# Kernel optimization log

Measured on AMD Instinct MI355X. Metric: run time of the kernel, lower is better.

Reference implementation:

```python
import jax, jax.numpy as jnp
import numpy as np

B, S, D = 4, 2048, 1024  # batch, seq_len, model dim (= qk_dim = output_dim)


def setup_inputs() -> dict:
    key = jax.random.key(0)
    kq, kk, kv, kwq, kwk, kwv = jax.random.split(key, 6)
    q = jax.random.normal(kq, (B, S, D), dtype=jnp.float32)
    k = jax.random.normal(kk, (B, S, D), dtype=jnp.float32)
    v = jax.random.normal(kv, (B, S, D), dtype=jnp.float32)
    # causal mask, broadcast over batch
    mask = jnp.broadcast_to(jnp.tril(jnp.ones((S, S), dtype=bool)), (B, S, S))
    W_q = jax.random.uniform(kwq, (D, D), dtype=jnp.float32)
    W_k = jax.random.uniform(kwk, (D, D), dtype=jnp.float32)
    W_v = jax.random.uniform(kwv, (D, D), dtype=jnp.float32)
    return {"q": q, "k": k, "v": v, "mask": mask, "W_q": W_q, "W_k": W_k, "W_v": W_v}


def reference(q, k, v, mask, W_q, W_k, W_v):
    q1 = q @ W_q  # (B, S, D)
    k1 = k @ W_k  # (B, S, D)
    v1 = v @ W_v  # (B, S, D)
    qk = jnp.einsum('bij,bkj->bik', q1, k1)  # (B, S, S)
    qk = qk * jax.lax.rsqrt(float(k1.shape[-1]))
    neg_inf = jnp.finfo(jnp.float32).min
    qk = jnp.where(mask, qk, neg_inf)
    s = jax.nn.softmax(qk, axis=-1)
    return jnp.einsum('bij,bjk->bik', s, v1)
```

## Files before the change

kernel.cpp:

```cpp
#include <hip/hip_runtime.h>
#include <hip/hip_bf16.h>
#include <float.h>


typedef __attribute__((ext_vector_type(8))) short bf16x8;
typedef __attribute__((ext_vector_type(4))) float f32x4;

#define MFMA16 __builtin_amdgcn_mfma_f32_16x16x32_bf16

union U8 { bf16x8 v; unsigned w[4]; };

__device__ __forceinline__ ushort f2bf(float x) {
  union { float f; unsigned u; } v; v.f = x;
  unsigned r = v.u + 0x7fffu + ((v.u >> 16) & 1u);
  return (ushort)(r >> 16);
}
__device__ __forceinline__ float bf2f(ushort h) {
  union { unsigned u; float f; } v; v.u = ((unsigned)h) << 16;
  return v.f;
}
__device__ __forceinline__ void splitf(float x, ushort& hi, ushort& lo) {
  hi = f2bf(x);
  lo = f2bf(x - bf2f(hi));
}

__device__ __forceinline__ bf16x8 cvt8(const float* lp) {
  U8 H;
#pragma unroll
  for (int p = 0; p < 4; ++p) {
    const unsigned u0 = __float_as_uint(lp[2 * p]);
    const unsigned u1 = __float_as_uint(lp[2 * p + 1]);
    const unsigned r0 = (u0 + 0x7fffu + ((u0 >> 16) & 1u)) >> 16;
    const unsigned r1 = (u1 + 0x7fffu + ((u1 >> 16) & 1u)) & 0xffff0000u;
    H.w[p] = r0 | r1;
  }
  return H.v;
}

#define GLOAD16(gp, lp)                                                        \
  __builtin_amdgcn_global_load_lds(                                            \
      (const __attribute__((address_space(1))) void*)(gp),                     \
      (__attribute__((address_space(3))) void*)(lp), 16, 0, 0)

__device__ __forceinline__ void stage_bf16_32(const ushort* g, int pitch,
                                              ushort* lds, int w, int lane) {
#pragma unroll
  for (int i = 0; i < 2; ++i) {
    const int c = w * 2 + i;
    const int row = c * 16 + (lane >> 2);
    const int kp = (lane & 3) * 8;
    GLOAD16(g + (size_t)row * pitch + kp, lds + c * 512);
  }
}
__device__ __forceinline__ void stage_bf16_64(const ushort* g, int pitch,
                                              ushort* lds, int w, int lane) {
#pragma unroll
  for (int i = 0; i < 4; ++i) {
    const int c = w * 4 + i;
    const int row = c * 8 + (lane >> 3);
    const int kp = (lane & 7) * 8;
    GLOAD16(g + (size_t)row * pitch + kp, lds + c * 512);
  }
}
__device__ __forceinline__ void stage_bf16_64x64(const ushort* g, int pitch,
                                                 ushort* lds, int w, int lane) {
#pragma unroll
  for (int i = 0; i < 2; ++i) {
    const int c = w * 2 + i;
    const int row = c * 8 + (lane >> 3);
    const int kp = (lane & 7) * 8;
    GLOAD16(g + (size_t)row * pitch + kp, lds + c * 512);
  }
}
__device__ __forceinline__ void stage_f32_32(const float* g, int pitch,
                                             float* lds, int w, int lane) {
#pragma unroll
  for (int i = 0; i < 4; ++i) {
    const int c = w * 4 + i;
    const int row = c * 8 + (lane >> 3);
    const int kp = (lane & 7) * 4;
    GLOAD16(g + (size_t)row * pitch + kp, lds + c * 256);
  }
}

__global__ __launch_bounds__(256) void wt_split(
    const float* __restrict__ q, const float* __restrict__ k,
    const float* __restrict__ W0, const float* __restrict__ W1,
    const float* __restrict__ W2, ushort* __restrict__ Th0,
    ushort* __restrict__ Tl0, ushort* __restrict__ Th1,
    ushort* __restrict__ Tl1, ushort* __restrict__ Th2,
    ushort* __restrict__ qh, ushort* __restrict__ ql,
    ushort* __restrict__ kh, ushort* __restrict__ kl) {
  __shared__ float t[32][33];
  const int f = blockIdx.x;
  if (f < 3072) {
    const int z = f >> 10, r10 = f & 1023;
    const int bx = r10 & 31, by = r10 >> 5;
    const float* W = z == 0 ? W0 : (z == 1 ? W1 : W2);
    ushort* Th = z == 0 ? Th0 : (z == 1 ? Th1 : Th2);
    ushort* Tl = z == 0 ? Tl0 : (z == 1 ? Tl1 : nullptr);
    const int r = threadIdx.x >> 3, c4 = (threadIdx.x & 7) * 4;
    const float4 x = *reinterpret_cast<const float4*>(
        &W[(size_t)(bx * 32 + r) * 1024 + by * 32 + c4]);
    t[r][c4] = x.x; t[r][c4 + 1] = x.y; t[r][c4 + 2] = x.z; t[r][c4 + 3] = x.w;
    __syncthreads();
    ushort h[4], l[4];
#pragma unroll
    for (int j = 0; j < 4; ++j) splitf(t[c4 + j][r], h[j], l[j]);
    const size_t o = (size_t)(by * 32 + r) * 1024 + bx * 32 + c4;
    *reinterpret_cast<ushort4*>(&Th[o]) = ushort4{h[0], h[1], h[2], h[3]};
    if (Tl)
      *reinterpret_cast<ushort4*>(&Tl[o]) = ushort4{l[0], l[1], l[2], l[3]};
  } else {
    const int fl = f - 3072;
    const float* X = (fl >> 11) ? k : q;
    ushort* H = (fl >> 11) ? kh : qh;
    ushort* L = (fl >> 11) ? kl : ql;
    const int n4 = 2097152;
    for (int i = (fl & 2047) * 256 + threadIdx.x; i < n4; i += 2048 * 256) {
      const float4 x = reinterpret_cast<const float4*>(X)[i];
      ushort h0, l0, h1, l1, h2, l2, h3, l3;
      splitf(x.x, h0, l0); splitf(x.y, h1, l1);
      splitf(x.z, h2, l2); splitf(x.w, h3, l3);
      reinterpret_cast<ushort4*>(H)[i] = ushort4{h0, h1, h2, h3};
      reinterpret_cast<ushort4*>(L)[i] = ushort4{l0, l1, l2, l3};
    }
  }
}

__global__ __launch_bounds__(256) void proj_qk(
    const ushort* __restrict__ Ah0, const ushort* __restrict__ Al0,
    const ushort* __restrict__ Ah1, const ushort* __restrict__ Al1,
    const ushort* __restrict__ Bh0, const ushort* __restrict__ Bl0,
    const ushort* __restrict__ Bh1, const ushort* __restrict__ Bl1,
    ushort* __restrict__ Oh0, ushort* __restrict__ Ol0,
    ushort* __restrict__ Oh1, ushort* __restrict__ Ol1) {
  __shared__ ushort Ahs[4096], Als[4096], Bhs[4096], Bls[4096];
  const int f = blockIdx.x;
  const int xb = (f >> 3) & 7;
  const int r = (f & 7) + ((f >> 6) << 3);
  const int yb = r & 63, z = r >> 6;
  const ushort* Ah = z ? Ah1 : Ah0;
  const ushort* Al = z ? Al1 : Al0;
  const ushort* Bh = z ? Bh1 : Bh0;
  const ushort* Bl = z ? Bl1 : Bl0;
  ushort* Oh = z ? Oh1 : Oh0;
  ushort* Ol = z ? Ol1 : Ol0;
  const int tid = threadIdx.x, lane = tid & 63, w = tid >> 6;
  const int wr = w >> 1, wc = w & 1;
  const int lr = lane & 15, kg = lane >> 4;
  const int m0 = yb * 128, n0 = xb * 128;
  f32x4 acc[4][4] = {};

  for (int k0 = 0; k0 < 1024; k0 += 32) {
    stage_bf16_32(Ah + (size_t)m0 * 1024 + k0, 1024, Ahs, w, lane);
    stage_bf16_32(Al + (size_t)m0 * 1024 + k0, 1024, Als, w, lane);
    stage_bf16_32(Bh + (size_t)n0 * 1024 + k0, 1024, Bhs, w, lane);
    stage_bf16_32(Bl + (size_t)n0 * 1024 + k0, 1024, Bls, w, lane);
    __syncthreads();
    bf16x8 ah[4], al[4], bh[4], bl[4];
#pragma unroll
    for (int m = 0; m < 4; ++m) {
      ah[m] = *reinterpret_cast<bf16x8*>(&Ahs[(wr * 64 + m * 16 + lr) * 32 + kg * 8]);
      al[m] = *reinterpret_cast<bf16x8*>(&Als[(wr * 64 + m * 16 + lr) * 32 + kg * 8]);
    }
#pragma unroll
    for (int n = 0; n < 4; ++n) {
      bh[n] = *reinterpret_cast<bf16x8*>(&Bhs[(wc * 64 + n * 16 + lr) * 32 + kg * 8]);
      bl[n] = *reinterpret_cast<bf16x8*>(&Bls[(wc * 64 + n * 16 + lr) * 32 + kg * 8]);
    }
#pragma unroll
    for (int m = 0; m < 4; ++m)
#pragma unroll
      for (int n = 0; n < 4; ++n) {
        acc[m][n] = MFMA16(ah[m], bh[n], acc[m][n], 0, 0, 0);
        acc[m][n] = MFMA16(ah[m], bl[n], acc[m][n], 0, 0, 0);
        acc[m][n] = MFMA16(al[m], bh[n], acc[m][n], 0, 0, 0);
      }
    __syncthreads();
  }
#pragma unroll
  for (int m = 0; m < 4; ++m)
#pragma unroll
    for (int n = 0; n < 4; ++n)
#pragma unroll
      for (int reg = 0; reg < 4; ++reg) {
        const int gm = m0 + wr * 64 + m * 16 + kg * 4 + reg;
        const int gn = n0 + wc * 64 + n * 16 + lr;
        ushort h, l;
        splitf(acc[m][n][reg], h, l);
        Oh[(size_t)gm * 1024 + gn] = h;
        Ol[(size_t)gm * 1024 + gn] = l;
      }
}

__global__ __launch_bounds__(256) void qk2(
    const ushort* __restrict__ q1h, const ushort* __restrict__ q1l,
    const ushort* __restrict__ k1h, const ushort* __restrict__ k1l,
    float* __restrict__ scoresA, float* __restrict__ scoresB) {
  __shared__ ushort Ahs[4096], Als[4096], Bhs[4096], Bls[4096];
  const int f = blockIdx.x;
  const int s = (f & 7) * 136 + (f >> 3);
  const int z = s / 544;
  const int rem = s % 544;
  const int b = rem / 136;
  int p = rem % 136, ti = 0, accp = 0;
  while (accp + ti + 1 <= p) { accp += ti + 1; ++ti; }
  const int tj = p - accp;
  const int tid = threadIdx.x, lane = tid & 63, w = tid >> 6;
  const int wr = w >> 1, wc = w & 1;
  const int lr = lane & 15, kg = lane >> 4;
  const int kh0 = z * 512;
  const ushort* qh = q1h + ((size_t)b * 2048 + ti * 128) * 1024 + kh0;
  const ushort* ql = q1l + ((size_t)b * 2048 + ti * 128) * 1024 + kh0;
  const ushort* kh = k1h + ((size_t)b * 2048 + tj * 128) * 1024 + kh0;
  const ushort* kl = k1l + ((size_t)b * 2048 + tj * 128) * 1024 + kh0;
  f32x4 acc[4][4] = {};

  for (int k0 = 0; k0 < 512; k0 += 32) {
    stage_bf16_32(qh + k0, 1024, Ahs, w, lane);
    stage_bf16_32(ql + k0, 1024, Als, w, lane);
    stage_bf16_32(kh + k0, 1024, Bhs, w, lane);
    stage_bf16_32(kl + k0, 1024, Bls, w, lane);
    __syncthreads();
    bf16x8 ah[4], al[4], bh[4], bl[4];
#pragma unroll
    for (int m = 0; m < 4; ++m) {
      ah[m] = *reinterpret_cast<bf16x8*>(&Ahs[(wr * 64 + m * 16 + lr) * 32 + kg * 8]);
      al[m] = *reinterpret_cast<bf16x8*>(&Als[(wr * 64 + m * 16 + lr) * 32 + kg * 8]);
    }
#pragma unroll
    for (int n = 0; n < 4; ++n) {
      bh[n] = *reinterpret_cast<bf16x8*>(&Bhs[(wc * 64 + n * 16 + lr) * 32 + kg * 8]);
      bl[n] = *reinterpret_cast<bf16x8*>(&Bls[(wc * 64 + n * 16 + lr) * 32 + kg * 8]);
    }
#pragma unroll
    for (int m = 0; m < 4; ++m)
#pragma unroll
      for (int n = 0; n < 4; ++n) {
        acc[m][n] = MFMA16(ah[m], bh[n], acc[m][n], 0, 0, 0);
        acc[m][n] = MFMA16(ah[m], bl[n], acc[m][n], 0, 0, 0);
        acc[m][n] = MFMA16(al[m], bh[n], acc[m][n], 0, 0, 0);
      }
    __syncthreads();
  }
  const float sc = 0.03125f;
  float* st = (z ? scoresB : scoresA) + ((size_t)b * 136 + p) * 16384;
#pragma unroll
  for (int m = 0; m < 4; ++m)
#pragma unroll
    for (int n = 0; n < 4; ++n)
#pragma unroll
      for (int reg = 0; reg < 4; ++reg) {
        const int il = wr * 64 + m * 16 + kg * 4 + reg;
        const int jl = wc * 64 + n * 16 + lr;
        st[il * 128 + jl] = acc[m][n][reg] * sc;
      }
}

__global__ __launch_bounds__(256) void sm_projv(
    float* __restrict__ scoresA, const float* __restrict__ scoresB,
    const ushort* __restrict__ Wvt, const float* __restrict__ V,
    ushort* __restrict__ v1t) {
  __shared__ __align__(16) char smem[24576];
  const int tid = threadIdx.x, lane = tid & 63, w = tid >> 6;
  const int fg = blockIdx.x;
  if (fg < 8192) {
    float* red = reinterpret_cast<float*>(smem);
    const int b = fg >> 11, r = fg & 2047;
    const int ti = r >> 7, rl = r & 127, ncol = (ti + 1) * 128;
    const int valid = r + 1;
    const size_t tbase = ((size_t)b * 136 + (ti * (ti + 1)) / 2) * 16384;
    float* srowA = scoresA + tbase;
    const float* srowB = scoresB + tbase;

    float vals[2][4];
    float mx = -FLT_MAX;
#pragma unroll
    for (int c = 0; c < 2; ++c) {
      const int j = tid * 4 + c * 1024;
      const size_t o = (size_t)(j >> 7) * 16384 + rl * 128 + (j & 127);
      const float4 a = *reinterpret_cast<const float4*>(srowA + o);
      const float4 bb = *reinterpret_cast<const float4*>(srowB + o);
      vals[c][0] = (j + 0 < valid) ? a.x + bb.x : -FLT_MAX;
      vals[c][1] = (j + 1 < valid) ? a.y + bb.y : -FLT_MAX;
      vals[c][2] = (j + 2 < valid) ? a.z + bb.z : -FLT_MAX;
      vals[c][3] = (j + 3 < valid) ? a.w + bb.w : -FLT_MAX;
      mx = fmaxf(mx, fmaxf(fmaxf(vals[c][0], vals[c][1]),
                           fmaxf(vals[c][2], vals[c][3])));
    }
#pragma unroll
    for (int o = 32; o; o >>= 1) mx = fmaxf(mx, __shfl_xor(mx, o));
    if (lane == 0) red[w] = mx;
    __syncthreads();
    mx = fmaxf(fmaxf(red[0], red[1]), fmaxf(red[2], red[3]));

    float ex[2][4];
    float sum = 0.f;
#pragma unroll
    for (int c = 0; c < 2; ++c)
#pragma unroll
      for (int e = 0; e < 4; ++e) {
        const int j = tid * 4 + c * 1024 + e;
        ex[c][e] = (j < valid) ? __expf(vals[c][e] - mx) : 0.f;
        sum += ex[c][e];
      }
#pragma unroll
    for (int o = 32; o; o >>= 1) sum += __shfl_xor(sum, o);
    if (lane == 0) red[4 + w] = sum;
    __syncthreads();
    sum = red[4] + red[5] + red[6] + red[7];
    const float inv = 1.f / sum;
#pragma unroll
    for (int c = 0; c < 2; ++c) {
      const int j = tid * 4 + c * 1024;
      if (j < ncol) {
        ushort* pt =
            reinterpret_cast<ushort*>(srowA + (size_t)(j >> 7) * 16384);
        ushort4 pw;
        pw.x = f2bf(ex[c][0] * inv); pw.y = f2bf(ex[c][1] * inv);
        pw.z = f2bf(ex[c][2] * inv); pw.w = f2bf(ex[c][3] * inv);
        *reinterpret_cast<ushort4*>(&pt[rl * 256 + (j & 127)]) = pw;
      }
    }
  } else {
    ushort* Ahs = reinterpret_cast<ushort*>(smem);
    float* Bs = reinterpret_cast<float*>(smem + 8192);
    const int f2 = fg - 8192;
    const int yb = (f2 >> 3) & 7;
    const int xb = (f2 & 7) + ((f2 >> 6) << 3);
    const int wr = w >> 1, wc = w & 1;
    const int lr = lane & 15, kg = lane >> 4;
    const int m0 = yb * 128;
    const int n0 = xb * 128;
    f32x4 acc[4][4] = {};

    for (int k0 = 0; k0 < 1024; k0 += 32) {
      stage_bf16_32(Wvt + (size_t)m0 * 1024 + k0, 1024, Ahs, w, lane);
      stage_f32_32(V + (size_t)n0 * 1024 + k0, 1024, Bs, w, lane);
      __syncthreads();
      bf16x8 ah[4], bh[4];
#pragma unroll
      for (int m = 0; m < 4; ++m)
        ah[m] = *reinterpret_cast<bf16x8*>(
            &Ahs[(wr * 64 + m * 16 + lr) * 32 + kg * 8]);
#pragma unroll
      for (int n = 0; n < 4; ++n)
        bh[n] = cvt8(&Bs[(wc * 64 + n * 16 + lr) * 32 + kg * 8]);
#pragma unroll
      for (int m = 0; m < 4; ++m)
#pragma unroll
        for (int n = 0; n < 4; ++n)
          acc[m][n] = MFMA16(ah[m], bh[n], acc[m][n], 0, 0, 0);
      __syncthreads();
    }
#pragma unroll
    for (int m = 0; m < 4; ++m)
#pragma unroll
      for (int n = 0; n < 4; ++n)
#pragma unroll
        for (int reg = 0; reg < 4; ++reg) {
          const int gm = m0 + wr * 64 + m * 16 + kg * 4 + reg;
          const int gn = n0 + wc * 64 + n * 16 + lr;
          const int b = gn >> 11, jj = gn & 2047;
          v1t[((size_t)b << 21) + (size_t)gm * 2048 + jj] = f2bf(acc[m][n][reg]);
        }
  }
}

__global__ __launch_bounds__(256) void pv2(const float* __restrict__ scores,
                                           const ushort* __restrict__ v1t,
                                           float* __restrict__ out) {
  __shared__ ushort Ps[128 * 64], Vs[64 * 64];
  const int fl = blockIdx.x;
  const int s = (fl & 7) * 128 + (fl >> 3);
  const int b = s >> 8, rem = s & 255;
  const int ti = 15 - (rem >> 4);
  const int n0 = (rem & 15) * 64;
  const int tid = threadIdx.x, lane = tid & 63, w = tid >> 6;
  const int wr = w >> 1, wc = w & 1;
  const int lr = lane & 15, kg = lane >> 4;
  const int tri_ti = (ti * (ti + 1)) / 2;
  const ushort* vbase = v1t + ((size_t)b << 21) + (size_t)n0 * 2048;
  const int kend = (ti + 1) * 128;
  f32x4 acc[4][2] = {};

  for (int k0 = 0; k0 < kend; k0 += 64) {
    const ushort* pt = reinterpret_cast<const ushort*>(
        scores + ((size_t)b * 136 + tri_ti + (k0 >> 7)) * 16384);
    stage_bf16_64(pt + (k0 & 64), 256, Ps, w, lane);
    stage_bf16_64x64(vbase + k0, 2048, Vs, w, lane);
    __syncthreads();
#pragma unroll
    for (int t2 = 0; t2 < 2; ++t2) {
      bf16x8 pa[4], vb[2];
#pragma unroll
      for (int m = 0; m < 4; ++m)
        pa[m] = *reinterpret_cast<bf16x8*>(
            &Ps[(wr * 64 + m * 16 + lr) * 64 + t2 * 32 + kg * 8]);
#pragma unroll
      for (int n = 0; n < 2; ++n)
        vb[n] = *reinterpret_cast<bf16x8*>(
            &Vs[(wc * 32 + n * 16 + lr) * 64 + t2 * 32 + kg * 8]);
#pragma unroll
      for (int m = 0; m < 4; ++m)
#pragma unroll
        for (int n = 0; n < 2; ++n)
          acc[m][n] = MFMA16(pa[m], vb[n], acc[m][n], 0, 0, 0);
    }
    __syncthreads();
  }
#pragma unroll
  for (int m = 0; m < 4; ++m)
#pragma unroll
    for (int n = 0; n < 2; ++n)
#pragma unroll
      for (int reg = 0; reg < 4; ++reg) {
        const int gm = ti * 128 + wr * 64 + m * 16 + kg * 4 + reg;
        const int gn = n0 + wc * 32 + n * 16 + lr;
        out[((size_t)b * 2048 + gm) * 1024 + gn] = acc[m][n][reg];
      }
}

extern "C" void kernel_launch(void* const* d_in, const int* in_sizes, int n_in,
                              void* d_out, int out_size, void* d_ws,
                              size_t ws_size, hipStream_t stream) {
  const float* q = (const float*)d_in[0];
  const float* k = (const float*)d_in[1];
  const float* v = (const float*)d_in[2];
  const float* Wq = (const float*)d_in[4];
  const float* Wk = (const float*)d_in[5];
  const float* Wv = (const float*)d_in[6];
  float* out = (float*)d_out;

  char* ws = (char*)d_ws;
  const size_t SCORES_T = 35651584;
  float* scoresA = (float*)ws;
  float* scoresB = (float*)(ws + SCORES_T);
  ushort* qsh = (ushort*)ws;
  ushort* qsl = qsh + 8388608;
  ushort* ksh = qsh + 2 * 8388608;
  ushort* ksl = qsh + 3 * 8388608;
  ushort* q1hi = (ushort*)(ws + 2 * SCORES_T);
  ushort* q1lo = q1hi + 8388608;
  ushort* k1hi = q1hi + 2 * 8388608;
  ushort* k1lo = q1hi + 3 * 8388608;
  ushort* v1t = (ushort*)(ws + 2 * SCORES_T);
  ushort* Wqth = (ushort*)(ws + 2 * SCORES_T + 67108864);
  ushort* Wqtl = Wqth + 1048576;
  ushort* Wkth = Wqth + 2097152;
  ushort* Wktl = Wqth + 3145728;
  ushort* Wvt  = Wqth + 4194304;
  const size_t need = 2 * SCORES_T + 67108864 + 10485760;
  if (ws_size < need) return;

  dim3 blk(256);
  wt_split<<<dim3(7168), blk, 0, stream>>>(q, k, Wq, Wk, Wv, Wqth, Wqtl, Wkth,
                                           Wktl, Wvt, qsh, qsl, ksh, ksl);
  proj_qk<<<dim3(1024), blk, 0, stream>>>(qsh, qsl, ksh, ksl, Wqth, Wqtl,
                                          Wkth, Wktl, q1hi, q1lo, k1hi, k1lo);
  qk2<<<dim3(1088), blk, 0, stream>>>(q1hi, q1lo, k1hi, k1lo, scoresA,
                                      scoresB);
  sm_projv<<<dim3(8704), blk, 0, stream>>>(scoresA, scoresB, Wvt, v, v1t);
  pv2<<<dim3(1024), blk, 0, stream>>>(scoresA, v1t, out);
}
```

Before: 312.6 us.

## Rewrite Q/K projection GEMM as 256x256 double-buffered 8-wave pipelined kernel

Replaces the 128x128, 4-wave projection GEMM with a 256x256-tile, 512-thread kernel. It streams the three split-bf16 products (hi*hi, lo*hi, hi*lo) as three sequential K segments through double-buffered, XOR-swizzled LDS using async global-to-LDS loads. Staging is interleaved with MFMA quadrants under fine-grained barriers, vmcnt waits and raised wave priority, to overlap memory traffic with compute and cut redundant operand loads. The cost is a much larger LDS footprint (two waves-per-SIMD target) and fewer blocks (256), which may underfill the CUs. Correctness also depends on the hand-placed waitcnt and barrier ordering.

```diff
diff --git a/kernel.cpp b/kernel.cpp
--- a/kernel.cpp
+++ b/kernel.cpp
@@ -42,6 +42,9 @@
       (const __attribute__((address_space(1))) void*)(gp),                     \
       (__attribute__((address_space(3))) void*)(lp), 16, 0, 0)
 
+#define BARRIER() asm volatile("s_barrier" ::: "memory")
+#define VMCNT4() asm volatile("s_waitcnt vmcnt(4)" ::: "memory")
+
 __device__ __forceinline__ void stage_bf16_32(const ushort* g, int pitch,
                                               ushort* lds, int w, int lane) {
 #pragma unroll
@@ -80,6 +83,18 @@
     const int row = c * 8 + (lane >> 3);
     const int kp = (lane & 7) * 4;
     GLOAD16(g + (size_t)row * pitch + kp, lds + c * 256);
+  }
+}
+
+__device__ __forceinline__ void stage_half8(const ushort* __restrict__ g,
+                                            ushort* lds, int k0, int t) {
+#pragma unroll
+  for (int i = 0; i < 2; ++i) {
+    const int c = t + i * 512;
+    const int row = c >> 3;
+    const int pcb = (c & 7) * 16;
+    const int lcb = pcb ^ (((row >> 2) & 3) << 5);
+    GLOAD16(g + (size_t)row * 1024 + k0 + (lcb >> 1), lds + c * 8);
   }
 }
 
@@ -128,65 +143,136 @@
   }
 }
 
-__global__ __launch_bounds__(256) void proj_qk(
+__global__ __launch_bounds__(512, 2) void proj_qk8(
     const ushort* __restrict__ Ah0, const ushort* __restrict__ Al0,
     const ushort* __restrict__ Ah1, const ushort* __restrict__ Al1,
     const ushort* __restrict__ Bh0, const ushort* __restrict__ Bl0,
     const ushort* __restrict__ Bh1, const ushort* __restrict__ Bl1,
     ushort* __restrict__ Oh0, ushort* __restrict__ Ol0,
     ushort* __restrict__ Oh1, ushort* __restrict__ Ol1) {
-  __shared__ ushort Ahs[4096], Als[4096], Bhs[4096], Bls[4096];
-  const int f = blockIdx.x;
-  const int xb = (f >> 3) & 7;
-  const int r = (f & 7) + ((f >> 6) << 3);
-  const int yb = r & 63, z = r >> 6;
+  __shared__ ushort As[2][16384];
+  __shared__ ushort Bs[2][16384];
+  const int bid = blockIdx.x;
+  const int fid = (bid & 7) * 32 + (bid >> 3);
+  const int z = fid >> 7, r = fid & 127;
+  const int yt = r >> 2, xt = r & 3;
   const ushort* Ah = z ? Ah1 : Ah0;
   const ushort* Al = z ? Al1 : Al0;
   const ushort* Bh = z ? Bh1 : Bh0;
   const ushort* Bl = z ? Bl1 : Bl0;
   ushort* Oh = z ? Oh1 : Oh0;
   ushort* Ol = z ? Ol1 : Ol0;
-  const int tid = threadIdx.x, lane = tid & 63, w = tid >> 6;
-  const int wr = w >> 1, wc = w & 1;
+  const size_t am0 = (size_t)yt * 256 * 1024;
+  const size_t bn0 = (size_t)xt * 256 * 1024;
+  const int t = threadIdx.x;
+  const int lane = t & 63, w = t >> 6;
+  const int wm = w >> 2, wn = w & 3;
   const int lr = lane & 15, kg = lane >> 4;
-  const int m0 = yb * 128, n0 = xb * 128;
-  f32x4 acc[4][4] = {};
-
-  for (int k0 = 0; k0 < 1024; k0 += 32) {
-    stage_bf16_32(Ah + (size_t)m0 * 1024 + k0, 1024, Ahs, w, lane);
-    stage_bf16_32(Al + (size_t)m0 * 1024 + k0, 1024, Als, w, lane);
-    stage_bf16_32(Bh + (size_t)n0 * 1024 + k0, 1024, Bhs, w, lane);
-    stage_bf16_32(Bl + (size_t)n0 * 1024 + k0, 1024, Bls, w, lane);
-    __syncthreads();
-    bf16x8 ah[4], al[4], bh[4], bl[4];
-#pragma unroll
-    for (int m = 0; m < 4; ++m) {
-      ah[m] = *reinterpret_cast<bf16x8*>(&Ahs[(wr * 64 + m * 16 + lr) * 32 + kg * 8]);
-      al[m] = *reinterpret_cast<bf16x8*>(&Als[(wr * 64 + m * 16 + lr) * 32 + kg * 8]);
-    }
-#pragma unroll
-    for (int n = 0; n < 4; ++n) {
-      bh[n] = *reinterpret_cast<bf16x8*>(&Bhs[(wc * 64 + n * 16 + lr) * 32 + kg * 8]);
-      bl[n] = *reinterpret_cast<bf16x8*>(&Bls[(wc * 64 + n * 16 + lr) * 32 + kg * 8]);
-    }
+  f32x4 acc[8][4] = {};
+  bf16x8 Ar[4][2], Br[4][2];
+
+  auto stage_unit = [&](int kt, int u) {
+    if (kt >= 48) kt -= 48;
+    const int seg = kt >> 4;
+    const int k0 = (kt & 15) * 64;
+    const int slot = kt & 1;
+    const int h = u & 1;
+    if (u < 2) {
+      const ushort* g = ((seg == 1) ? Al : Ah) + am0 + (size_t)(h * 128) * 1024;
+      stage_half8(g, &As[slot][h * 8192], k0, t);
+    } else {
+      const ushort* g = ((seg == 2) ? Bl : Bh) + bn0 + (size_t)(h * 128) * 1024;
+      stage_half8(g, &Bs[slot][h * 8192], k0, t);
+    }
+  };
+  auto loadA = [&](int slot, int mq) {
 #pragma unroll
     for (int m = 0; m < 4; ++m)
 #pragma unroll
-      for (int n = 0; n < 4; ++n) {
-        acc[m][n] = MFMA16(ah[m], bh[n], acc[m][n], 0, 0, 0);
-        acc[m][n] = MFMA16(ah[m], bl[n], acc[m][n], 0, 0, 0);
-        acc[m][n] = MFMA16(al[m], bh[n], acc[m][n], 0, 0, 0);
-      }
-    __syncthreads();
-  }
-#pragma unroll
-  for (int m = 0; m < 4; ++m)
+      for (int ks = 0; ks < 2; ++ks) {
+        const int row = wm * 128 + (mq * 4 + m) * 16 + lr;
+        const int cb = (ks * 64 + kg * 16) ^ (((row >> 2) & 3) << 5);
+        Ar[m][ks] =
+            *reinterpret_cast<const bf16x8*>(&As[slot][row * 64 + (cb >> 1)]);
+      }
+  };
+  auto loadB = [&](int slot, int nq) {
+#pragma unroll
+    for (int n = 0; n < 2; ++n)
+#pragma unroll
+      for (int ks = 0; ks < 2; ++ks) {
+        const int col = wn * 64 + (nq * 2 + n) * 16 + lr;
+        const int cb = (ks * 64 + kg * 16) ^ (((col >> 2) & 3) << 5);
+        Br[nq * 2 + n][ks] =
+            *reinterpret_cast<const bf16x8*>(&Bs[slot][col * 64 + (cb >> 1)]);
+      }
+  };
+  auto mfma_q = [&](int mq, int nq) {
+    __builtin_amdgcn_s_setprio(1);
+#pragma unroll
+    for (int m = 0; m < 4; ++m)
+#pragma unroll
+      for (int n = 0; n < 2; ++n)
+#pragma unroll
+        for (int ks = 0; ks < 2; ++ks)
+          acc[mq * 4 + m][nq * 2 + n] = MFMA16(
+              Ar[m][ks], Br[nq * 2 + n][ks], acc[mq * 4 + m][nq * 2 + n], 0, 0, 0);
+    __builtin_amdgcn_s_setprio(0);
+  };
+
+  stage_unit(0, 0); stage_unit(0, 1); stage_unit(0, 2); stage_unit(0, 3);
+  stage_unit(1, 0);
+
+  for (int it = 0; it < 24; ++it) {
+    const int kt1 = 2 * it + 1;
+    stage_unit(kt1, 1);
+    VMCNT4(); BARRIER();
+    loadA(0, 0); loadB(0, 0);
+    mfma_q(0, 0);
+    BARRIER();
+    stage_unit(kt1, 2);
+    BARRIER();
+    loadB(0, 1);
+    mfma_q(0, 1);
+    BARRIER();
+    stage_unit(kt1, 3);
+    BARRIER();
+    loadA(0, 1);
+    mfma_q(1, 0);
+    BARRIER();
+    stage_unit(kt1 + 1, 0);
+    BARRIER();
+    mfma_q(1, 1);
+    BARRIER();
+    stage_unit(kt1 + 1, 1);
+    VMCNT4(); BARRIER();
+    loadA(1, 0); loadB(1, 0);
+    mfma_q(0, 0);
+    BARRIER();
+    stage_unit(kt1 + 1, 2);
+    BARRIER();
+    loadB(1, 1);
+    mfma_q(0, 1);
+    BARRIER();
+    stage_unit(kt1 + 1, 3);
+    BARRIER();
+    loadA(1, 1);
+    mfma_q(1, 0);
+    BARRIER();
+    stage_unit(kt1 + 2, 0);
+    BARRIER();
+    mfma_q(1, 1);
+    BARRIER();
+  }
+
+#pragma unroll
+  for (int m = 0; m < 8; ++m)
 #pragma unroll
     for (int n = 0; n < 4; ++n)
 #pragma unroll
       for (int reg = 0; reg < 4; ++reg) {
-        const int gm = m0 + wr * 64 + m * 16 + kg * 4 + reg;
-        const int gn = n0 + wc * 64 + n * 16 + lr;
+        const int gm = yt * 256 + wm * 128 + m * 16 + kg * 4 + reg;
+        const int gn = xt * 256 + wn * 64 + n * 16 + lr;
         ushort h, l;
         splitf(acc[m][n][reg], h, l);
         Oh[(size_t)gm * 1024 + gn] = h;
@@ -457,8 +543,9 @@
   dim3 blk(256);
   wt_split<<<dim3(7168), blk, 0, stream>>>(q, k, Wq, Wk, Wv, Wqth, Wqtl, Wkth,
                                            Wktl, Wvt, qsh, qsl, ksh, ksl);
-  proj_qk<<<dim3(1024), blk, 0, stream>>>(qsh, qsl, ksh, ksl, Wqth, Wqtl,
-                                          Wkth, Wktl, q1hi, q1lo, k1hi, k1lo);
+  proj_qk8<<<dim3(256), dim3(512), 0, stream>>>(qsh, qsl, ksh, ksl, Wqth,
+                                                Wqtl, Wkth, Wktl, q1hi, q1lo,
+                                                k1hi, k1lo);
   qk2<<<dim3(1088), blk, 0, stream>>>(q1hi, q1lo, k1hi, k1lo, scoresA,
                                       scoresB);
   sm_projv<<<dim3(8704), blk, 0, stream>>>(scoresA, scoresB, Wvt, v, v1t);
```

Measured after the change: 316.6 us. Within noise of the previous version (+1.3%).
